# Optimization experiments

Hardware: AMD Instinct MI355X
Metric: run time of the kernel (lower is better)

The kernel has to match this reference:

```python
import jax, jax.numpy as jnp
import numpy as np

N, E, DIN, DOUT = 50000, 800000, 64, 64


def setup_inputs() -> dict:
    key = jax.random.key(0)
    ks = jax.random.split(key, 24)
    x = jax.random.normal(ks[0], (N, DIN), dtype=jnp.float32)
    edge_index = jax.random.randint(ks[1], (2, E), 0, N, dtype=jnp.int64)
    s = 1.0 / np.sqrt(DIN)
    sg = 1.0 / np.sqrt(DOUT)
    def lin(k, fan_in, shape, scale):
        return jax.random.uniform(k, shape, jnp.float32, -scale, scale)
    inp = {"x": x, "edge_index": edge_index}
    names = ["hp", "lp", "i", "hp2", "lp2"]
    for j, nm in enumerate(names):
        inp[f"W_{nm}"] = lin(ks[2 + 4 * j], DIN, (DIN, DOUT), s)
        inp[f"b_{nm}"] = lin(ks[3 + 4 * j], DIN, (DOUT,), s)
        inp[f"wa_{nm}"] = lin(ks[4 + 4 * j], DOUT, (DOUT, 1), sg)
        inp[f"ba_{nm}"] = lin(ks[5 + 4 * j], DOUT, (1,), sg)
    return inp


def _mean_agg(x, src, dst, inv_deg):
    # mean aggregation: (D^-1 A) x, via gather + segment scatter-add
    agg = jax.ops.segment_sum(x[src], dst, num_segments=N)
    return agg * inv_deg[:, None]


def reference(x, edge_index, W_hp, b_hp, W_lp, b_lp, W_i, b_i,
              W_hp2, b_hp2, W_lp2, b_lp2,
              wa_hp, ba_hp, wa_lp, ba_lp, wa_i, ba_i,
              wa_hp2, ba_hp2, wa_lp2, ba_lp2):
    src, dst = edge_index[0], edge_index[1]
    deg = jax.ops.segment_sum(jnp.ones((E,), x.dtype), dst, num_segments=N)
    inv_deg = 1.0 / jnp.maximum(deg, 1.0)

    ax = _mean_agg(x, src, dst, inv_deg)          # A_hat x
    aax = _mean_agg(ax, src, dst, inv_deg)
    P = {
        "i": x,
        "lp": ax,
        "hp": x - ax,
        "lp2": aax,
        "hp2": x - 2.0 * ax + aax,
    }
    Ws = {"hp": (W_hp, b_hp), "lp": (W_lp, b_lp), "i": (W_i, b_i),
          "hp2": (W_hp2, b_hp2), "lp2": (W_lp2, b_lp2)}
    gates = {"hp": (wa_hp, ba_hp), "lp": (wa_lp, ba_lp), "i": (wa_i, ba_i),
             "hp2": (wa_hp2, ba_hp2), "lp2": (wa_lp2, ba_lp2)}

    out = jnp.zeros((N, DOUT), x.dtype)
    for nm in ["hp", "lp", "hp2", "lp2", "i"]:
        W, b = Ws[nm]
        H = jax.nn.relu(P[nm] @ W + b)            # [N, DOUT]
        wa, ba = gates[nm]
        alpha = jax.nn.sigmoid(H @ wa + ba)[:, 0]  # [N]
        # diag(alpha) @ H == alpha[:, None] * H
        out = out + alpha[:, None] * H
    return out
```

## Files before the change

### kernel.cpp

```cpp
#include <hip/hip_runtime.h>
#include <hip/hip_bf16.h>

constexpr int N = 50000;
constexpr int E = 800000;
constexpr int D = 64;
constexpr int GSZ = N / 8;
constexpr int SLOTS = 64;
constexpr int ZB = 49;
constexpr int PB = 1563;
constexpr int EBLK = E / 256;

typedef __attribute__((ext_vector_type(8))) short s8v;
typedef __attribute__((ext_vector_type(4))) float f32x4;

struct BranchParams {
  const float* W[5];
  const float* b[5];
  const float* wa[5];
  const float* ba[5];
};

__device__ __forceinline__ short f2bf(float f) {
  unsigned u = __float_as_uint(f);
  u += 0x7fff + ((u >> 16) & 1);
  return (short)(u >> 16);
}
__device__ __forceinline__ float bflo(unsigned v) { return __uint_as_float(v << 16); }
__device__ __forceinline__ float bfhi(unsigned v) { return __uint_as_float(v & 0xffff0000u); }
__device__ __forceinline__ float bfs(short s) {
  return __uint_as_float(((unsigned)(unsigned short)s) << 16);
}
__device__ __forceinline__ unsigned pack2(float lo, float hi) {
  return ((unsigned)(unsigned short)f2bf(lo)) |
         (((unsigned)(unsigned short)f2bf(hi)) << 16);
}

__device__ __forceinline__ void prepw_frag(const BranchParams& P,
                                           short* __restrict__ wf,
                                           int bfrag, int lane) {
  int br = bfrag >> 3, ct = (bfrag >> 1) & 3, kk = bfrag & 1;
  const float* W = P.W[br];
  int col = ct * 16 + (lane & 15);
  int k0 = kk * 32 + (lane >> 4) * 8;
  s8v v;
#pragma unroll
  for (int j = 0; j < 8; ++j) v[j] = f2bf(W[(k0 + j) * D + col]);
  ((s8v*)wf)[bfrag * 64 + lane] = v;
}

__global__ __launch_bounds__(256) void k_zero_prep(
    int* __restrict__ pos, const float* __restrict__ x,
    uint* __restrict__ xbf, BranchParams P, short* __restrict__ wf) {
  int b = blockIdx.x;
  if (b < ZB) {
    int t = b * 256 + threadIdx.x;
    if (t < N / 4) ((int4*)pos)[t] = int4{0, 0, 0, 0};
  } else if (b < ZB + PB) {
    int t = (b - ZB) * 256 + threadIdx.x;
    if (t < N * D / 8) {
      const float4* p = (const float4*)(x + (size_t)t * 8);
      float4 a = p[0], c = p[1];
      uint4 o;
      o.x = pack2(a.x, a.y);
      o.y = pack2(a.z, a.w);
      o.z = pack2(c.x, c.y);
      o.w = pack2(c.z, c.w);
      ((uint4*)xbf)[t] = o;
    }
  } else {
    int wid = threadIdx.x >> 6, lane = threadIdx.x & 63;
    for (int bfrag = wid; bfrag < 40; bfrag += 4) prepw_frag(P, wf, bfrag, lane);
  }
}

__global__ __launch_bounds__(256) void k_fill8(const int* __restrict__ ei,
                                               int* __restrict__ pos,
                                               ushort* __restrict__ srcs) {
  int g = blockIdx.x & 7;
  int e = (blockIdx.x >> 3) * 256 + threadIdx.x;
  int dst = ei[E + e];
  if ((unsigned)(dst - g * GSZ) < (unsigned)GSZ) {
    int slot = atomicAdd(&pos[dst], 1);
    if (slot < SLOTS) srcs[dst * SLOTS + slot] = (ushort)ei[e];
  }
}

__global__ __launch_bounds__(256) void k_agg(
    const int* __restrict__ pos, const ushort* __restrict__ srcs,
    const uint* __restrict__ inbf, uint* __restrict__ outbf) {
  int node = blockIdx.x * 4 + (threadIdx.x >> 6);
  int lane = threadIdx.x & 63;
  int half = lane >> 5;
  int fp = lane & 31;
  int deg = pos[node];
  int m = min(deg, SLOTS);
  int start = node * SLOTS;
  int end = start + m;
  int np = m >> 1;
  float sx0 = 0.f, sy0 = 0.f, sx1 = 0.f, sy1 = 0.f;
  float sx2 = 0.f, sy2 = 0.f, sx3 = 0.f, sy3 = 0.f;
  int e = start + half;
  int i = 0;
  for (; i + 4 <= np; i += 4, e += 8) {
    int s0 = srcs[e], s1 = srcs[e + 2], s2 = srcs[e + 4], s3 = srcs[e + 6];
    uint v0 = inbf[s0 * 32 + fp];
    uint v1 = inbf[s1 * 32 + fp];
    uint v2 = inbf[s2 * 32 + fp];
    uint v3 = inbf[s3 * 32 + fp];
    sx0 += bflo(v0); sy0 += bfhi(v0);
    sx1 += bflo(v1); sy1 += bfhi(v1);
    sx2 += bflo(v2); sy2 += bfhi(v2);
    sx3 += bflo(v3); sy3 += bfhi(v3);
  }
  for (; i < np; ++i, e += 2) {
    int s0 = srcs[e];
    uint v0 = inbf[s0 * 32 + fp];
    sx0 += bflo(v0); sy0 += bfhi(v0);
  }
  if ((m & 1) && half == 0) {
    int s0 = srcs[end - 1];
    uint v0 = inbf[s0 * 32 + fp];
    sx0 += bflo(v0); sy0 += bfhi(v0);
  }
  float sx = (sx0 + sx1) + (sx2 + sx3);
  float sy = (sy0 + sy1) + (sy2 + sy3);
  sx += __shfl_xor(sx, 32);
  sy += __shfl_xor(sy, 32);
  if (half == 0) {
    float inv = 1.0f / fmaxf((float)deg, 1.0f);
    outbf[node * 32 + fp] = pack2(sx * inv, sy * inv);
  }
}

__device__ __forceinline__ void branch_wave(
    const ushort* __restrict__ xbf, const ushort* __restrict__ axbf,
    const ushort* __restrict__ aaxbf, const BranchParams& P,
    const short* __restrict__ wf, float* __restrict__ out,
    int base, int lane) {
  const int l16 = lane & 15;
  const int kg = lane >> 4;

  const s8v* xr = (const s8v*)(xbf + (size_t)(base + l16) * D);
  const s8v* ar = (const s8v*)(axbf + (size_t)(base + l16) * D);
  const s8v* cr = (const s8v*)(aaxbf + (size_t)(base + l16) * D);
  s8v xv[2], av[2], bv[2];
  xv[0] = xr[kg]; xv[1] = xr[4 + kg];
  av[0] = ar[kg]; av[1] = ar[4 + kg];
  bv[0] = cr[kg]; bv[1] = cr[4 + kg];

  s8v hpv[2], hp2v[2];
#pragma unroll
  for (int kk = 0; kk < 2; ++kk) {
#pragma unroll
    for (int j = 0; j < 8; ++j) {
      float fx = bfs(xv[kk][j]), fa = bfs(av[kk][j]), fb = bfs(bv[kk][j]);
      hpv[kk][j] = f2bf(fx - fa);
      hp2v[kk][j] = f2bf(fx - 2.0f * fa + fb);
    }
  }

  f32x4 oacc[4] = {{0.f, 0.f, 0.f, 0.f}, {0.f, 0.f, 0.f, 0.f},
                   {0.f, 0.f, 0.f, 0.f}, {0.f, 0.f, 0.f, 0.f}};
  const s8v* wf8 = (const s8v*)wf;

#pragma unroll
  for (int brn = 0; brn < 5; ++brn) {
    s8v a0, a1;
    switch (brn) {
      case 0: a0 = hpv[0]; a1 = hpv[1]; break;
      case 1: a0 = av[0]; a1 = av[1]; break;
      case 2: a0 = xv[0]; a1 = xv[1]; break;
      case 3: a0 = hp2v[0]; a1 = hp2v[1]; break;
      default: a0 = bv[0]; a1 = bv[1]; break;
    }
    f32x4 acc[4];
#pragma unroll
    for (int ct = 0; ct < 4; ++ct) {
      f32x4 a = {0.f, 0.f, 0.f, 0.f};
      a = __builtin_amdgcn_mfma_f32_16x16x32_bf16(
          a0, wf8[((brn * 4 + ct) * 2 + 0) * 64 + lane], a, 0, 0, 0);
      a = __builtin_amdgcn_mfma_f32_16x16x32_bf16(
          a1, wf8[((brn * 4 + ct) * 2 + 1) * 64 + lane], a, 0, 0, 0);
      acc[ct] = a;
    }
    float bcol[4], wacol[4];
#pragma unroll
    for (int ct = 0; ct < 4; ++ct) {
      bcol[ct] = P.b[brn][ct * 16 + l16];
      wacol[ct] = P.wa[brn][ct * 16 + l16];
    }
    const float bav = P.ba[brn][0];
#pragma unroll
    for (int i = 0; i < 4; ++i) {
      float h[4], gg = 0.f;
#pragma unroll
      for (int ct = 0; ct < 4; ++ct) {
        h[ct] = fmaxf(acc[ct][i] + bcol[ct], 0.f);
        gg = fmaf(h[ct], wacol[ct], gg);
      }
#pragma unroll
      for (int o = 1; o < 16; o <<= 1) gg += __shfl_xor(gg, o);
      float alpha = 1.0f / (1.0f + __expf(-(gg + bav)));
#pragma unroll
      for (int ct = 0; ct < 4; ++ct) oacc[ct][i] = fmaf(alpha, h[ct], oacc[ct][i]);
    }
  }
#pragma unroll
  for (int ct = 0; ct < 4; ++ct)
#pragma unroll
    for (int i = 0; i < 4; ++i)
      out[(size_t)(base + kg * 4 + i) * D + ct * 16 + l16] = oacc[ct][i];
}

__global__ __launch_bounds__(256) void k_branch(
    const ushort* __restrict__ xbf, const ushort* __restrict__ axbf,
    const ushort* __restrict__ aaxbf, BranchParams P,
    const short* __restrict__ wf, float* __restrict__ out) {
  const int waveId = blockIdx.x * 4 + (threadIdx.x >> 6);
  if (waveId >= N / 16) return;
  branch_wave(xbf, axbf, aaxbf, P, wf, out, waveId * 16, threadIdx.x & 63);
}

extern "C" void kernel_launch(void* const* d_in, const int* in_sizes, int n_in,
                              void* d_out, int out_size, void* d_ws, size_t ws_size,
                              hipStream_t stream) {
  const float* x = (const float*)d_in[0];
  const int* ei = (const int*)d_in[1];
  BranchParams P;
  for (int i = 0; i < 5; ++i) {
    P.W[i] = (const float*)d_in[2 + 4 * i];
    P.b[i] = (const float*)d_in[3 + 4 * i];
    P.wa[i] = (const float*)d_in[4 + 4 * i];
    P.ba[i] = (const float*)d_in[5 + 4 * i];
  }

  char* w = (char*)d_ws;
  uint* xbf = (uint*)w;     w += (size_t)N * D * 2;
  uint* axbf = (uint*)w;    w += (size_t)N * D * 2;
  uint* aaxbf = (uint*)w;   w += (size_t)N * D * 2;
  int* pos = (int*)w;       w += (size_t)N * 4;
  ushort* srcs = (ushort*)w; w += (size_t)N * SLOTS * 2;
  short* wf = (short*)w;

  hipLaunchKernelGGL(k_zero_prep, dim3(ZB + PB + 1), dim3(256), 0, stream,
                     pos, x, xbf, P, wf);
  hipLaunchKernelGGL(k_fill8, dim3(EBLK * 8), dim3(256), 0, stream, ei, pos, srcs);
  hipLaunchKernelGGL(k_agg, dim3(N / 4), dim3(256), 0, stream, pos, srcs, xbf, axbf);
  hipLaunchKernelGGL(k_agg, dim3(N / 4), dim3(256), 0, stream, pos, srcs, axbf, aaxbf);
  hipLaunchKernelGGL(k_branch, dim3((N / 16 + 3) / 4), dim3(256), 0, stream,
                     (const ushort*)xbf, (const ushort*)axbf, (const ushort*)aaxbf,
                     P, wf, (float*)d_out);
}
```

Measured before the change: 117.8 us.

## Fuse second aggregation into branch kernel via LDS and merge fill with prep

The second mean aggregation now runs inside the branch kernel. Each 256-thread block aggregates 16 nodes into shared memory, and then one wave runs the MFMA branch computation on them, so the aax buffer no longer makes a round trip through global memory. Zeroing is split into its own small kernel, and the bf16 conversion, weight prep and edge-slot fill are merged into one launch. As a trade-off, three of the four waves sit idle during the MFMA phase, which lowers parallelism in that part of the fused kernel.

```diff
diff --git a/kernel.cpp b/kernel.cpp
--- a/kernel.cpp
+++ b/kernel.cpp
@@ -9,6 +9,7 @@
 constexpr int ZB = 49;
 constexpr int PB = 1563;
 constexpr int EBLK = E / 256;
+constexpr int LSTR = 36;
 
 typedef __attribute__((ext_vector_type(8))) short s8v;
 typedef __attribute__((ext_vector_type(4))) float f32x4;
@@ -48,15 +49,21 @@
   ((s8v*)wf)[bfrag * 64 + lane] = v;
 }
 
-__global__ __launch_bounds__(256) void k_zero_prep(
-    int* __restrict__ pos, const float* __restrict__ x,
+__global__ __launch_bounds__(256) void k_zero(int4* __restrict__ pos4) {
+  int t = blockIdx.x * 256 + threadIdx.x;
+  if (t < N / 4) pos4[t] = int4{0, 0, 0, 0};
+}
+
+__global__ __launch_bounds__(256) void k_fill_prep(
+    const int* __restrict__ ei, int* __restrict__ pos,
+    ushort* __restrict__ srcs, const float* __restrict__ x,
     uint* __restrict__ xbf, BranchParams P, short* __restrict__ wf) {
   int b = blockIdx.x;
-  if (b < ZB) {
-    int t = b * 256 + threadIdx.x;
-    if (t < N / 4) ((int4*)pos)[t] = int4{0, 0, 0, 0};
-  } else if (b < ZB + PB) {
-    int t = (b - ZB) * 256 + threadIdx.x;
+  if (b == 0) {
+    int wid = threadIdx.x >> 6, lane = threadIdx.x & 63;
+    for (int bfrag = wid; bfrag < 40; bfrag += 4) prepw_frag(P, wf, bfrag, lane);
+  } else if (b <= PB) {
+    int t = (b - 1) * 256 + threadIdx.x;
     if (t < N * D / 8) {
       const float4* p = (const float4*)(x + (size_t)t * 8);
       float4 a = p[0], c = p[1];
@@ -68,28 +75,20 @@
       ((uint4*)xbf)[t] = o;
     }
   } else {
-    int wid = threadIdx.x >> 6, lane = threadIdx.x & 63;
-    for (int bfrag = wid; bfrag < 40; bfrag += 4) prepw_frag(P, wf, bfrag, lane);
-  }
-}
-
-__global__ __launch_bounds__(256) void k_fill8(const int* __restrict__ ei,
-                                               int* __restrict__ pos,
-                                               ushort* __restrict__ srcs) {
-  int g = blockIdx.x & 7;
-  int e = (blockIdx.x >> 3) * 256 + threadIdx.x;
-  int dst = ei[E + e];
-  if ((unsigned)(dst - g * GSZ) < (unsigned)GSZ) {
-    int slot = atomicAdd(&pos[dst], 1);
-    if (slot < SLOTS) srcs[dst * SLOTS + slot] = (ushort)ei[e];
-  }
-}
-
-__global__ __launch_bounds__(256) void k_agg(
+    int fb = b - 1 - PB;
+    int g = fb & 7;
+    int e = (fb >> 3) * 256 + threadIdx.x;
+    int dst = ei[E + e];
+    if ((unsigned)(dst - g * GSZ) < (unsigned)GSZ) {
+      int slot = atomicAdd(&pos[dst], 1);
+      if (slot < SLOTS) srcs[dst * SLOTS + slot] = (ushort)ei[e];
+    }
+  }
+}
+
+__device__ __forceinline__ uint agg_row(
     const int* __restrict__ pos, const ushort* __restrict__ srcs,
-    const uint* __restrict__ inbf, uint* __restrict__ outbf) {
-  int node = blockIdx.x * 4 + (threadIdx.x >> 6);
-  int lane = threadIdx.x & 63;
+    const uint* __restrict__ inbf, int node, int lane) {
   int half = lane >> 5;
   int fp = lane & 31;
   int deg = pos[node];
@@ -126,23 +125,42 @@
   float sy = (sy0 + sy1) + (sy2 + sy3);
   sx += __shfl_xor(sx, 32);
   sy += __shfl_xor(sy, 32);
-  if (half == 0) {
-    float inv = 1.0f / fmaxf((float)deg, 1.0f);
-    outbf[node * 32 + fp] = pack2(sx * inv, sy * inv);
-  }
-}
-
-__device__ __forceinline__ void branch_wave(
-    const ushort* __restrict__ xbf, const ushort* __restrict__ axbf,
-    const ushort* __restrict__ aaxbf, const BranchParams& P,
-    const short* __restrict__ wf, float* __restrict__ out,
-    int base, int lane) {
+  float inv = 1.0f / fmaxf((float)deg, 1.0f);
+  return pack2(sx * inv, sy * inv);
+}
+
+__global__ __launch_bounds__(256) void k_agg(
+    const int* __restrict__ pos, const ushort* __restrict__ srcs,
+    const uint* __restrict__ inbf, uint* __restrict__ outbf) {
+  int node = blockIdx.x * 4 + (threadIdx.x >> 6);
+  int lane = threadIdx.x & 63;
+  uint r = agg_row(pos, srcs, inbf, node, lane);
+  if ((lane >> 5) == 0) outbf[node * 32 + (lane & 31)] = r;
+}
+
+__global__ __launch_bounds__(256) void k_agg2_branch(
+    const int* __restrict__ pos, const ushort* __restrict__ srcs,
+    const uint* __restrict__ axbf, const ushort* __restrict__ xbf,
+    BranchParams P, const short* __restrict__ wf, float* __restrict__ out) {
+  __shared__ uint aaxl[16 * LSTR];
+  const int lane = threadIdx.x & 63;
+  const int wid = threadIdx.x >> 6;
+  const int base = blockIdx.x * 16;
+
+  for (int j = 0; j < 4; ++j) {
+    int dl = wid * 4 + j;
+    uint r = agg_row(pos, srcs, axbf, base + dl, lane);
+    if ((lane >> 5) == 0) aaxl[dl * LSTR + (lane & 31)] = r;
+  }
+  __syncthreads();
+  if (wid != 0) return;
+
   const int l16 = lane & 15;
   const int kg = lane >> 4;
 
   const s8v* xr = (const s8v*)(xbf + (size_t)(base + l16) * D);
-  const s8v* ar = (const s8v*)(axbf + (size_t)(base + l16) * D);
-  const s8v* cr = (const s8v*)(aaxbf + (size_t)(base + l16) * D);
+  const s8v* ar = (const s8v*)((const ushort*)axbf + (size_t)(base + l16) * D);
+  const s8v* cr = (const s8v*)(aaxl + l16 * LSTR);
   s8v xv[2], av[2], bv[2];
   xv[0] = xr[kg]; xv[1] = xr[4 + kg];
   av[0] = ar[kg]; av[1] = ar[4 + kg];
@@ -210,15 +228,6 @@
 #pragma unroll
     for (int i = 0; i < 4; ++i)
       out[(size_t)(base + kg * 4 + i) * D + ct * 16 + l16] = oacc[ct][i];
-}
-
-__global__ __launch_bounds__(256) void k_branch(
-    const ushort* __restrict__ xbf, const ushort* __restrict__ axbf,
-    const ushort* __restrict__ aaxbf, BranchParams P,
-    const short* __restrict__ wf, float* __restrict__ out) {
-  const int waveId = blockIdx.x * 4 + (threadIdx.x >> 6);
-  if (waveId >= N / 16) return;
-  branch_wave(xbf, axbf, aaxbf, P, wf, out, waveId * 16, threadIdx.x & 63);
 }
 
 extern "C" void kernel_launch(void* const* d_in, const int* in_sizes, int n_in,
@@ -235,19 +244,16 @@
   }
 
   char* w = (char*)d_ws;
-  uint* xbf = (uint*)w;     w += (size_t)N * D * 2;
-  uint* axbf = (uint*)w;    w += (size_t)N * D * 2;
-  uint* aaxbf = (uint*)w;   w += (size_t)N * D * 2;
-  int* pos = (int*)w;       w += (size_t)N * 4;
+  uint* xbf = (uint*)w;      w += (size_t)N * D * 2;
+  uint* axbf = (uint*)w;     w += (size_t)N * D * 2;
+  int* pos = (int*)w;        w += (size_t)N * 4;
   ushort* srcs = (ushort*)w; w += (size_t)N * SLOTS * 2;
   short* wf = (short*)w;
 
-  hipLaunchKernelGGL(k_zero_prep, dim3(ZB + PB + 1), dim3(256), 0, stream,
-                     pos, x, xbf, P, wf);
-  hipLaunchKernelGGL(k_fill8, dim3(EBLK * 8), dim3(256), 0, stream, ei, pos, srcs);
+  hipLaunchKernelGGL(k_zero, dim3(ZB), dim3(256), 0, stream, (int4*)pos);
+  hipLaunchKernelGGL(k_fill_prep, dim3(1 + PB + 8 * EBLK), dim3(256), 0, stream,
+                     ei, pos, srcs, x, xbf, P, wf);
   hipLaunchKernelGGL(k_agg, dim3(N / 4), dim3(256), 0, stream, pos, srcs, xbf, axbf);
-  hipLaunchKernelGGL(k_agg, dim3(N / 4), dim3(256), 0, stream, pos, srcs, axbf, aaxbf);
-  hipLaunchKernelGGL(k_branch, dim3((N / 16 + 3) / 4), dim3(256), 0, stream,
-                     (const ushort*)xbf, (const ushort*)axbf, (const ushort*)aaxbf,
-                     P, wf, (float*)d_out);
-}
+  hipLaunchKernelGGL(k_agg2_branch, dim3(N / 16), dim3(256), 0, stream,
+                     pos, srcs, axbf, (const ushort*)xbf, P, wf, (float*)d_out);
+}
```

After: 125.6 us. +6.6%, slower.
